# Performance work log

Measured on AMD Instinct MI355X. Metric: run time of the kernel, lower is better.

The kernel has to match this reference:

```python
import jax, jax.numpy as jnp
import numpy as np

N = 131072          # number of items ranked in one soft_rank call
CAPACITY = 3.0      # self.capcity in the torch module


def _pav_kl(y, w):
    """KL isotonic regression (non-increasing fit) via Pool-Adjacent-Violators.
    Pooled block value = logsumexp(y_block) - logsumexp(w_block).
    Matches torchsort / fast-soft-sort isotonic_kl. Sequential O(N)."""
    n = y.shape[0]

    def push(i, st):
        ly, lw, val, start, ptr = st
        ly = ly.at[ptr].set(y[i])
        lw = lw.at[ptr].set(w[i])
        val = val.at[ptr].set(y[i] - w[i])
        start = start.at[ptr].set(i)
        ptr = ptr + 1

        def cond(s):
            _, _, v, _, p = s
            return (p >= 2) & (v[p - 2] <= v[p - 1])

        def merge(s):
            ly, lw, v, stt, p = s
            ny = jnp.logaddexp(ly[p - 2], ly[p - 1])
            nw = jnp.logaddexp(lw[p - 2], lw[p - 1])
            return (ly.at[p - 2].set(ny), lw.at[p - 2].set(nw),
                    v.at[p - 2].set(ny - nw), stt, p - 1)

        return jax.lax.while_loop(cond, merge, (ly, lw, val, start, ptr))

    z = jnp.zeros((n,), y.dtype)
    st0 = (z, z, z, jnp.full((n,), n, jnp.int32), jnp.int32(0))
    ly, lw, val, start, ptr = jax.lax.fori_loop(0, n, push, st0)
    # invalidate stale stack slots, then map each element to its block value
    start = jnp.where(jnp.arange(n) < ptr, start, n)
    blk = jnp.searchsorted(start, jnp.arange(n), side='right') - 1
    return val[blk]


@jax.custom_vjp
def isotonic_kl(y, w):
    return _pav_kl(y, w)


def _iso_fwd(y, w):
    sol = _pav_kl(y, w)
    return sol, (y, w, sol)


def _iso_bwd(res, g):
    y, w, sol = res
    n = y.shape[0]
    # blocks = maximal runs of constant solution (exact equality by construction)
    blk = jnp.cumsum(jnp.concatenate([jnp.array([True]), sol[1:] != sol[:-1]])) - 1
    gsum = jax.ops.segment_sum(g, blk, num_segments=n)

    def seg_softmax(v):
        m = jax.ops.segment_max(v, blk, num_segments=n)
        lse = jnp.log(jax.ops.segment_sum(jnp.exp(v - m[blk]), blk, num_segments=n)) + m
        return jnp.exp(v - lse[blk])

    return seg_softmax(y) * gsum[blk], -seg_softmax(w) * gsum[blk]


isotonic_kl.defvjp(_iso_fwd, _iso_bwd)


def soft_rank_kl(scores):
    """torchsort.soft_rank(scores[None], regularization='kl'), strength=1, ascending."""
    n = scores.shape[0]
    w_log = jnp.log(jnp.arange(n, 0, -1, dtype=scores.dtype))  # log([n, ..., 1])
    perm = jnp.argsort(-scores)          # descending, stable
    s = scores[perm]
    sol = isotonic_kl(s, w_log)
    inv = jnp.argsort(perm)
    return jnp.exp(s - sol)[inv]


def setup_inputs() -> dict:
    key = jax.random.key(0)
    k = jax.random.split(key, 5)
    x = jax.random.normal(k[0], (N, 1), jnp.float32)
    # torch Linear default init bounds: 1/sqrt(fan_in)
    w1 = jax.random.uniform(k[1], (1, 32), jnp.float32, -1.0, 1.0)
    b1 = jax.random.uniform(k[2], (32,), jnp.float32, -1.0, 1.0)
    lim2 = 1.0 / np.sqrt(32.0)
    w2 = jax.random.uniform(k[3], (32, 1), jnp.float32, -lim2, lim2)
    b2 = jax.random.uniform(k[4], (1,), jnp.float32, -lim2, lim2)
    return {"x": x, "w1": w1, "b1": b1, "w2": w2, "b2": b2}


def reference(x, w1, b1, w2, b2):
    h = jnp.maximum(x @ w1 + b1, 0.0)            # [N, 32]
    scores = (h @ w2 + b2).reshape(-1)           # [N]
    ranks = soft_rank_kl(scores)                 # [N]
    other = jax.lax.stop_gradient(ranks) % CAPACITY
    ranks = (ranks - other) / CAPACITY + 1.0
    return ranks.reshape(-1, 1)
```

## Files before the change

kernel.cpp:

```cpp
#include <hip/hip_runtime.h>
#include <stdint.h>

typedef unsigned int u32;
typedef unsigned long long u64;

#define N_ITEMS 131072
#define NB 131072
#define NSLICE 4
#define MBLK 64
#define BUCK_PER_BLK 2048
#define CH_PER_BLK 32
#define PAD 65
#define REGSLOT 2048
#define FIXSCALE 268435456.0f
#define FIXMASK ((1ull << 46) - 1)


__device__ __forceinline__ float wsumf(int s, int e) {
  return 0.5f * (float)(e - s + 1) * (float)(2 * N_ITEMS - s - e);
}

__device__ __forceinline__ float key_to_score(u32 key) {
  u32 m = ~key;
  u32 u = (m & 0x80000000u) ? (m ^ 0x80000000u) : ~m;
  return __uint_as_float(u);
}

#define LOG2E 1.4426950408889634f
__device__ __forceinline__ float fexp(float x) { return exp2f(x * LOG2E); }

__device__ __forceinline__ u32 bucket_of(u32 key, u32 kmin, u32 kmax) {
  double scale = (double)NB / ((double)(kmax - kmin) + 1.0);
  u32 b = (u32)((double)(key - kmin) * scale);
  return b < NB ? b : (NB - 1);
}

__device__ __forceinline__ float recSY(int2 r) { return __int_as_float(r.y); }


__global__ __launch_bounds__(256) void score_key_kernel(
    const float* __restrict__ x,
    const float* __restrict__ w1, const float* __restrict__ b1,
    const float* __restrict__ w2, const float* __restrict__ b2,
    u32* __restrict__ keyRaw, u32* __restrict__ agg) {
  __shared__ u32 wmn[4], wmx[4];
  int t = threadIdx.x;
  int i = blockIdx.x * 256 + t;
  float xv = x[i];
  float s = b2[0];
#pragma unroll
  for (int j = 0; j < 32; ++j) {
    float h = fmaf(xv, w1[j], b1[j]);
    h = fmaxf(h, 0.0f);
    s = fmaf(h, w2[j], s);
  }
  u32 u = __float_as_uint(s);
  u32 m = u ^ ((u & 0x80000000u) ? 0xFFFFFFFFu : 0x80000000u);
  u32 key = ~m;
  keyRaw[i] = key;
  u32 mn = key, mx = key;
#pragma unroll
  for (int off = 32; off > 0; off >>= 1) {
    mn = min(mn, (u32)__shfl_xor((int)mn, off));
    mx = max(mx, (u32)__shfl_xor((int)mx, off));
  }
  if ((t & 63) == 0) { wmn[t >> 6] = mn; wmx[t >> 6] = mx; }
  __syncthreads();
  if (t == 0) {
    mn = min(min(wmn[0], wmn[1]), min(wmn[2], wmn[3]));
    mx = max(max(wmx[0], wmx[1]), max(wmx[2], wmx[3]));
    atomicMax(&agg[0], ~mn);
    atomicMax(&agg[1], mx);
  }
}


__global__ __launch_bounds__(256) void hist_kernel(
    const u32* __restrict__ keyRaw, const u32* __restrict__ agg,
    u64* __restrict__ hist8) {
  int t = threadIdx.x;
  int i = blockIdx.x * 256 + t;
  u32 kmin = ~agg[0], kmax = agg[1];
  u32 key = keyRaw[i];
  u32 g = bucket_of(key, kmin, kmax);
  float smax = key_to_score(kmin);
  float v = fexp(key_to_score(key) - smax);
  u64 fix = (u64)fmaxf(1.0f, fmaf(v, FIXSCALE, 0.5f));
  size_t slice = (size_t)(blockIdx.x & (NSLICE - 1)) * NB;
  atomicAdd(&hist8[slice + g], (1ull << 46) | fix);
}


__global__ __launch_bounds__(256) void solve_kernel(
    const u64* __restrict__ hist8, u64* __restrict__ flags, u64* __restrict__ flag2,
    u32* __restrict__ cdf, int2* __restrict__ REC,
    const u32* __restrict__ keyRaw, const u32* __restrict__ agg,
    float* __restrict__ out) {
  __shared__ u32 vals[BUCK_PER_BLK + 1];
  __shared__ float seL[BUCK_PER_BLK];
  __shared__ int   rST[CH_PER_BLK * PAD];
  __shared__ float rSY[CH_PER_BLK * PAD];
  __shared__ u32 sh[256];
  __shared__ u32 aggS[64];
  __shared__ u32 regS[65];
  __shared__ int lcnt[CH_PER_BLK];
  __shared__ int ca[16], cb[16], cM[16];
  __shared__ int shInt[4];
  int t = threadIdx.x, b = blockIdx.x;
  int B0 = b * BUCK_PER_BLK;
  for (int q = 0; q < 8; ++q) {
    int ii = q * 256 + t;
    u64 acc = 0;
#pragma unroll
    for (int c = 0; c < NSLICE; ++c) acc += hist8[(size_t)c * NB + B0 + ii];
    vals[ii] = (u32)(acc >> 46);
    seL[ii] = (float)(acc & FIXMASK) * (1.0f / FIXSCALE);
  }
  __syncthreads();
  u32 loc[8]; u32 s = 0;
  for (int q = 0; q < 8; ++q) { loc[q] = s; s += vals[t * 8 + q]; }
  sh[t] = s;
  __syncthreads();
  for (int off = 1; off < 256; off <<= 1) {
    u32 x2 = (t >= off) ? sh[t - off] : 0u;
    __syncthreads();
    sh[t] += x2;
    __syncthreads();
  }
  if (t == 0) atomicExch(&flags[b], (1ull << 32) | (u64)sh[255]);
  if (t < 64) {
    u64 f;
    do { f = atomicAdd(&flags[t], 0ull); } while ((u32)(f >> 32) == 0u);
    aggS[t] = (u32)f;
  }
  __syncthreads();
  if (t < 64) {
    u32 v = aggS[t];
    u32 inc = v;
    for (int off = 1; off < 64; off <<= 1) {
      u32 o2 = __shfl_up(inc, off);
      if (t >= off) inc += o2;
    }
    regS[t] = inc - v;
    if (t == 63) regS[64] = inc;
  }
  __syncthreads();
  u32 exclu = regS[b];
  u32 tbase = ((t == 0) ? 0u : sh[t - 1]) + exclu;
  u32 eb8[8];
  for (int q = 0; q < 8; ++q) { eb8[q] = tbase + loc[q]; vals[t * 8 + q] = eb8[q]; }
  {
    uint4* c4 = (uint4*)(cdf + B0 + t * 8);
    c4[0] = make_uint4(eb8[0], eb8[1], eb8[2], eb8[3]);
    c4[1] = make_uint4(eb8[4], eb8[5], eb8[6], eb8[7]);
  }
  if (t == 255) vals[BUCK_PER_BLK] = exclu + sh[255];
  __syncthreads();
  if (t < CH_PER_BLK) {
    int base = t * PAD;
    int ptr = 0; bool have = false;
    float syT = 0.0f; int stT = 0;
    for (int k = 0; k < 64; ++k) {
      u32 cs = vals[t * 64 + k], ce = vals[t * 64 + k + 1];
      if (ce == cs) continue;
      float syC = seL[t * 64 + k];
      int stC = (int)cs, eC = (int)ce - 1;
      while (have) {
        float SWc = wsumf(stC, eC);
        float SWt = wsumf(stT, stC - 1);
        if (!(syT * SWc <= syC * SWt)) break;
        syC += syT; stC = stT;
        if (ptr == 0) { have = false; break; }
        --ptr;
        stT = rST[base + ptr]; syT = rSY[base + ptr];
      }
      if (have) { rST[base + ptr] = stT; rSY[base + ptr] = syT; ++ptr; }
      stT = stC; syT = syC; have = true;
    }
    if (have) { rST[base + ptr] = stT; rSY[base + ptr] = syT; ++ptr; }
    lcnt[t] = ptr;
  }
  __syncthreads();
  for (int j = 0; j < 5; ++j) {
    int P = CH_PER_BLK >> (j + 1);
    if (t < P) {
      int p = t;
      int kL = p << (j + 1), kR = kL + (1 << j);
      int slotL = kL * PAD, slotR = kR * PAD;
      int nL = lcnt[kL], nR = lcnt[kR];
      int a = 0, bb = 0, hasM = 0;
      if (nL > 0 && nR > 0) {
        int gstartR = (int)vals[kR * 64];
        int gendR   = (int)vals[(kR + (1 << j)) * 64];
        float SYL = rSY[slotL + nL - 1]; int stL = rST[slotL + nL - 1];
        float SYR = rSY[slotR];
        int eR = (nR > 1) ? (rST[slotR + 1] - 1) : (gendR - 1);
        float SWL = wsumf(stL, gstartR - 1);
        float SWR = wsumf(gstartR, eR);
        if (SYL * SWR <= SYR * SWL) {
          hasM = 1;
          float SYM = SYL + SYR; int Ms = stL, Me = eR;
          a = 1; bb = 1;
          for (;;) {
            float SWM = wsumf(Ms, Me);
            if (a < nL) {
              float SYe = rSY[slotL + nL - 1 - a]; int ste = rST[slotL + nL - 1 - a];
              float SWe = wsumf(ste, Ms - 1);
              if (SYe * SWM <= SYM * SWe) { SYM += SYe; Ms = ste; ++a; continue; }
            }
            if (bb < nR) {
              float SYb = rSY[slotR + bb]; int sb = rST[slotR + bb];
              int eb = (bb + 1 < nR) ? (rST[slotR + bb + 1] - 1) : (gendR - 1);
              float SWb = wsumf(sb, eb);
              if (SYM * SWb <= SYb * SWM) { SYM += SYb; Me = eb; ++bb; continue; }
            }
            break;
          }
          rST[slotL + nL - a] = Ms; rSY[slotL + nL - a] = SYM;
        }
      }
      ca[p] = a; cb[p] = bb; cM[p] = hasM;
    }
    __syncthreads();
    {
      int w = t >> 6, lane = t & 63;
      for (int p = w; p < P; p += 4) {
        int kL = p << (j + 1), kR = kL + (1 << j);
        int nL = lcnt[kL], nR = lcnt[kR];
        int a = ca[p], bb = cb[p], hasM = cM[p];
        int destBase = kL * PAD + nL - a + hasM;
        int srcBase = kR * PAD + bb;
        int ncopy = nR - bb;
        for (int off = 0; off < ncopy; off += 64) {
          int k2 = off + lane; bool act = k2 < ncopy;
          int vt = 0; float vs = 0.f;
          if (act) { vt = rST[srcBase + k2]; vs = rSY[srcBase + k2]; }
          if (act) { rST[destBase + k2] = vt; rSY[destBase + k2] = vs; }
        }
      }
    }
    __syncthreads();
    if (t < P) {
      int p = t; int kL = p << (j + 1), kR = kL + (1 << j);
      lcnt[kL] = lcnt[kL] - ca[p] + cM[p] + (lcnt[kR] - cb[p]);
    }
    __syncthreads();
  }
  int myCnt = lcnt[0];
  for (int k = t; k < myCnt; k += 256)
    REC[(size_t)b * REGSLOT + k] = make_int2(rST[k], __float_as_int(rSY[k]));
  __syncthreads();
  int lvl = 0;
  for (;;) {
    if (b & (1 << lvl)) {
      __threadfence();
      if (t == 0) atomicExch(&flag2[b], (1ull << 32) | (u64)(u32)myCnt);
      break;
    }
    if (lvl == 6) {
      __threadfence();
      if (t == 0) atomicExch(&flag2[0], (2ull << 32) | (u64)(u32)myCnt);
      break;
    }
    int pb = b + (1 << lvl);
    if (t == 0) {
      u64 f;
      do { f = atomicAdd(&flag2[pb], 0ull); __builtin_amdgcn_s_sleep(1); } while ((f >> 32) == 0ull);
      shInt[0] = (int)(u32)f;
    }
    __syncthreads();
    __threadfence();
    int nR = shInt[0];
    int nL = myCnt;
    int slotL = b * REGSLOT, slotR = pb * REGSLOT;
    if (t == 0) {
      int a = 0, bb = 0, hasM = 0;
      if (nL > 0 && nR > 0) {
        int gstartR = (int)regS[pb];
        int gendR   = (int)regS[b + (2 << lvl)];
        int2 rL = REC[slotL + nL - 1];
        float SYL = recSY(rL); int stL = rL.x;
        int2 rR = REC[slotR];
        float SYR = recSY(rR);
        int eR = (nR > 1) ? (REC[slotR + 1].x - 1) : (gendR - 1);
        float SWL = wsumf(stL, gstartR - 1);
        float SWR = wsumf(gstartR, eR);
        if (SYL * SWR <= SYR * SWL) {
          hasM = 1;
          float SYM = SYL + SYR; int Ms = stL, Me = eR;
          a = 1; bb = 1;
          for (;;) {
            float SWM = wsumf(Ms, Me);
            if (a < nL) {
              int2 re = REC[slotL + nL - 1 - a];
              float SYe = recSY(re); int ste = re.x;
              float SWe = wsumf(ste, Ms - 1);
              if (SYe * SWM <= SYM * SWe) { SYM += SYe; Ms = ste; ++a; continue; }
            }
            if (bb < nR) {
              int2 rb = REC[slotR + bb];
              float SYb = recSY(rb); int sb = rb.x;
              int eb = (bb + 1 < nR) ? (REC[slotR + bb + 1].x - 1) : (gendR - 1);
              float SWb = wsumf(sb, eb);
              if (SYM * SWb <= SYb * SWM) { SYM += SYb; Me = eb; ++bb; continue; }
            }
            break;
          }
          REC[slotL + nL - a] = make_int2(Ms, __float_as_int(SYM));
        }
      }
      shInt[1] = a; shInt[2] = bb; shInt[3] = hasM;
    }
    __syncthreads();
    int a = shInt[1], bb = shInt[2], hasM = shInt[3];
    int destBase = slotL + nL - a + hasM;
    int srcBase = slotR + bb;
    int ncopy = nR - bb;
    for (int off = 0; off < ncopy; off += 256) {
      int k2 = off + t; bool act = k2 < ncopy;
      int2 vr = make_int2(0, 0);
      if (act) vr = REC[srcBase + k2];
      __syncthreads();
      if (act) REC[destBase + k2] = vr;
      __syncthreads();
    }
    __syncthreads();
    myCnt = nL - a + hasM + (nR - bb);
    ++lvl;
  }
  if (t == 0) {
    u64 f;
    do { f = atomicAdd(&flag2[0], 0ull); __builtin_amdgcn_s_sleep(2); } while ((f >> 32) != 2ull);
    shInt[0] = (int)(u32)f;
  }
  __syncthreads();
  __threadfence();
  int m = shInt[0];
  bool useL = (m <= CH_PER_BLK * PAD);
  if (useL) {
    for (int k = t; k < m; k += 256) {
      int2 r = REC[k];
      rST[k] = r.x; rSY[k] = __int_as_float(r.y);
    }
  }
  __syncthreads();
  u32 kmin = ~agg[0], kmax = agg[1];
  float smax = key_to_score(kmin);
  for (int q = 0; q < 8; ++q) {
    int i = b * 2048 + q * 256 + t;
    u32 key = keyRaw[i];
    u32 g = bucket_of(key, kmin, kmax);
    int p = (int)cdf[g];
    int lo = 0, hi = m - 1;
    if (useL) {
      while (lo < hi) {
        int mid = (lo + hi + 1) >> 1;
        if (rST[mid] <= p) lo = mid; else hi = mid - 1;
      }
      int s0 = rST[lo];
      int e0 = (lo + 1 < m) ? (rST[lo + 1] - 1) : (N_ITEMS - 1);
      float SW = wsumf(s0, e0);
      float sc = key_to_score(key);
      float rank = fexp(sc - smax) * SW / rSY[lo];
      out[i] = floorf(rank * (1.0f / 3.0f)) + 1.0f;
    } else {
      while (lo < hi) {
        int mid = (lo + hi + 1) >> 1;
        if (REC[mid].x <= p) lo = mid; else hi = mid - 1;
      }
      int2 r = REC[lo];
      int s0 = r.x;
      int e0 = (lo + 1 < m) ? (REC[lo + 1].x - 1) : (N_ITEMS - 1);
      float SW = wsumf(s0, e0);
      float sc = key_to_score(key);
      float rank = fexp(sc - smax) * SW / recSY(r);
      out[i] = floorf(rank * (1.0f / 3.0f)) + 1.0f;
    }
  }
}


extern "C" void kernel_launch(void* const* d_in, const int* in_sizes, int n_in,
                              void* d_out, int out_size, void* d_ws, size_t ws_size,
                              hipStream_t stream) {
  const float* x  = (const float*)d_in[0];
  const float* w1 = (const float*)d_in[1];
  const float* b1 = (const float*)d_in[2];
  const float* w2 = (const float*)d_in[3];
  const float* b2 = (const float*)d_in[4];
  float* out = (float*)d_out;

  char* ws = (char*)d_ws;
  size_t o = 0;
  u32* cdf    = (u32*)(ws + o); o += (size_t)(NB + 4) * 4;
  u32* keyRaw = (u32*)(ws + o); o += (size_t)N_ITEMS * 4;
  int2* REC   = (int2*)(ws + o); o += (size_t)N_ITEMS * 8;
  char* zbase = ws + o;
  u64* hist8  = (u64*)(ws + o); o += (size_t)NSLICE * NB * 8;
  u64* flags  = (u64*)(ws + o); o += (size_t)MBLK * 8;
  u64* flag2  = (u64*)(ws + o); o += (size_t)MBLK * 8;
  u32* agg    = (u32*)(ws + o); o += 64;
  size_t zbytes = (size_t)((ws + o) - zbase);

  hipMemsetAsync(zbase, 0, zbytes, stream);
  score_key_kernel<<<512, 256, 0, stream>>>(x, w1, b1, w2, b2, keyRaw, agg);
  hist_kernel<<<512, 256, 0, stream>>>(keyRaw, agg, hist8);
  solve_kernel<<<MBLK, 256, 0, stream>>>(hist8, flags, flag2, cdf, REC, keyRaw, agg, out);
}
```

Measured before the change: 142.9 us.

## Pad spin flags, use relaxed atomic loads, cache merge boundary records in LDS

```diff
diff --git a/kernel.cpp b/kernel.cpp
--- a/kernel.cpp
+++ b/kernel.cpp
@@ -12,6 +12,7 @@
 #define CH_PER_BLK 32
 #define PAD 65
 #define REGSLOT 2048
+#define FPAD 16
 #define FIXSCALE 268435456.0f
 #define FIXMASK ((1ull << 46) - 1)
 
@@ -37,15 +38,24 @@
 
 __device__ __forceinline__ float recSY(int2 r) { return __int_as_float(r.y); }
 
+__device__ __forceinline__ u64 agent_ld(const u64* p) {
+  return __hip_atomic_load(p, __ATOMIC_RELAXED, __HIP_MEMORY_SCOPE_AGENT);
+}
+
 
 __global__ __launch_bounds__(256) void score_key_kernel(
     const float* __restrict__ x,
     const float* __restrict__ w1, const float* __restrict__ b1,
     const float* __restrict__ w2, const float* __restrict__ b2,
-    u32* __restrict__ keyRaw, u32* __restrict__ agg) {
+    u32* __restrict__ keyRaw, u32* __restrict__ agg, u64* __restrict__ hist8) {
   __shared__ u32 wmn[4], wmx[4];
   int t = threadIdx.x;
   int i = blockIdx.x * 256 + t;
+  {
+    uint4 z = make_uint4(0u, 0u, 0u, 0u);
+    ((uint4*)hist8)[i] = z;
+    ((uint4*)hist8)[i + N_ITEMS] = z;
+  }
   float xv = x[i];
   float s = b2[0];
 #pragma unroll
@@ -127,10 +137,10 @@
     sh[t] += x2;
     __syncthreads();
   }
-  if (t == 0) atomicExch(&flags[b], (1ull << 32) | (u64)sh[255]);
+  if (t == 0) atomicExch(&flags[(size_t)b * FPAD], (1ull << 32) | (u64)sh[255]);
   if (t < 64) {
     u64 f;
-    do { f = atomicAdd(&flags[t], 0ull); } while ((u32)(f >> 32) == 0u);
+    do { f = agent_ld(&flags[(size_t)t * FPAD]); } while ((u32)(f >> 32) == 0u);
     aggS[t] = (u32)f;
   }
   __syncthreads();
@@ -250,11 +260,19 @@
   for (int k = t; k < myCnt; k += 256)
     REC[(size_t)b * REGSLOT + k] = make_int2(rST[k], __float_as_int(rSY[k]));
   __syncthreads();
+#define LRECC(idx_, st_, sy_) { int _a = (idx_); \
+    if (_a < 128) { st_ = rST[_a]; sy_ = rSY[_a]; } \
+    else { int2 _r = REC[slotL + nL - 1 - _a]; st_ = _r.x; sy_ = __int_as_float(_r.y); } }
+#define RRECC(idx_, st_, sy_) { int _i = (idx_); \
+    if (_i < 128) { st_ = rST[128 + _i]; sy_ = rSY[128 + _i]; } \
+    else { int2 _r = REC[slotR + _i]; st_ = _r.x; sy_ = __int_as_float(_r.y); } }
+#define RSTC(idx_, st_) { int _i = (idx_); \
+    if (_i < 128) { st_ = rST[128 + _i]; } else { st_ = REC[slotR + _i].x; } }
   int lvl = 0;
   for (;;) {
     if (b & (1 << lvl)) {
       __threadfence();
-      if (t == 0) atomicExch(&flag2[b], (1ull << 32) | (u64)(u32)myCnt);
+      if (t == 0) atomicExch(&flag2[(size_t)b * FPAD], (1ull << 32) | (u64)(u32)myCnt);
       break;
     }
     if (lvl == 6) {
@@ -263,26 +281,34 @@
       break;
     }
     int pb = b + (1 << lvl);
+    int nL = myCnt;
+    int slotL = b * REGSLOT, slotR = pb * REGSLOT;
+    if (t >= 64 && t < 192) {
+      int p2 = t - 64;
+      if (p2 < nL) { int2 r = REC[slotL + nL - 1 - p2]; rST[p2] = r.x; rSY[p2] = __int_as_float(r.y); }
+    }
     if (t == 0) {
       u64 f;
-      do { f = atomicAdd(&flag2[pb], 0ull); __builtin_amdgcn_s_sleep(1); } while ((f >> 32) == 0ull);
+      do { f = agent_ld(&flag2[(size_t)pb * FPAD]); __builtin_amdgcn_s_sleep(1); } while ((f >> 32) == 0ull);
       shInt[0] = (int)(u32)f;
     }
     __syncthreads();
     __threadfence();
     int nR = shInt[0];
-    int nL = myCnt;
-    int slotL = b * REGSLOT, slotR = pb * REGSLOT;
+    if (t >= 64 && t < 192) {
+      int p2 = t - 64;
+      if (p2 < nR) { int2 r = REC[slotR + p2]; rST[128 + p2] = r.x; rSY[128 + p2] = __int_as_float(r.y); }
+    }
+    __syncthreads();
     if (t == 0) {
       int a = 0, bb = 0, hasM = 0;
       if (nL > 0 && nR > 0) {
         int gstartR = (int)regS[pb];
         int gendR   = (int)regS[b + (2 << lvl)];
-        int2 rL = REC[slotL + nL - 1];
-        float SYL = recSY(rL); int stL = rL.x;
-        int2 rR = REC[slotR];
-        float SYR = recSY(rR);
-        int eR = (nR > 1) ? (REC[slotR + 1].x - 1) : (gendR - 1);
+        int stL; float SYL; LRECC(0, stL, SYL);
+        int sb0; float SYR; RRECC(0, sb0, SYR); (void)sb0;
+        int eR;
+        if (nR > 1) { int nx; RSTC(1, nx); eR = nx - 1; } else eR = gendR - 1;
         float SWL = wsumf(stL, gstartR - 1);
         float SWR = wsumf(gstartR, eR);
         if (SYL * SWR <= SYR * SWL) {
@@ -292,15 +318,14 @@
           for (;;) {
             float SWM = wsumf(Ms, Me);
             if (a < nL) {
-              int2 re = REC[slotL + nL - 1 - a];
-              float SYe = recSY(re); int ste = re.x;
+              int ste; float SYe; LRECC(a, ste, SYe);
               float SWe = wsumf(ste, Ms - 1);
               if (SYe * SWM <= SYM * SWe) { SYM += SYe; Ms = ste; ++a; continue; }
             }
             if (bb < nR) {
-              int2 rb = REC[slotR + bb];
-              float SYb = recSY(rb); int sb = rb.x;
-              int eb = (bb + 1 < nR) ? (REC[slotR + bb + 1].x - 1) : (gendR - 1);
+              int sb; float SYb; RRECC(bb, sb, SYb);
+              int eb;
+              if (bb + 1 < nR) { int nx; RSTC(bb + 1, nx); eb = nx - 1; } else eb = gendR - 1;
               float SWb = wsumf(sb, eb);
               if (SYM * SWb <= SYb * SWM) { SYM += SYb; Me = eb; ++bb; continue; }
             }
@@ -316,21 +341,33 @@
     int destBase = slotL + nL - a + hasM;
     int srcBase = slotR + bb;
     int ncopy = nR - bb;
-    for (int off = 0; off < ncopy; off += 256) {
-      int k2 = off + t; bool act = k2 < ncopy;
-      int2 vr = make_int2(0, 0);
-      if (act) vr = REC[srcBase + k2];
-      __syncthreads();
-      if (act) REC[destBase + k2] = vr;
-      __syncthreads();
+    if (destBase != srcBase) {
+      for (int off = 0; off < ncopy; off += 2048) {
+        int2 v[8];
+#pragma unroll
+        for (int j = 0; j < 8; ++j) {
+          int k2 = off + j * 256 + t;
+          if (k2 < ncopy) v[j] = REC[srcBase + k2];
+        }
+        __syncthreads();
+#pragma unroll
+        for (int j = 0; j < 8; ++j) {
+          int k2 = off + j * 256 + t;
+          if (k2 < ncopy) REC[destBase + k2] = v[j];
+        }
+        __syncthreads();
+      }
     }
     __syncthreads();
     myCnt = nL - a + hasM + (nR - bb);
     ++lvl;
   }
+#undef LRECC
+#undef RRECC
+#undef RSTC
   if (t == 0) {
     u64 f;
-    do { f = atomicAdd(&flag2[0], 0ull); __builtin_amdgcn_s_sleep(2); } while ((f >> 32) != 2ull);
+    do { f = agent_ld(&flag2[0]); __builtin_amdgcn_s_sleep(2); } while ((f >> 32) != 2ull);
     shInt[0] = (int)(u32)f;
   }
   __syncthreads();
@@ -395,15 +432,15 @@
   u32* cdf    = (u32*)(ws + o); o += (size_t)(NB + 4) * 4;
   u32* keyRaw = (u32*)(ws + o); o += (size_t)N_ITEMS * 4;
   int2* REC   = (int2*)(ws + o); o += (size_t)N_ITEMS * 8;
+  u64* hist8  = (u64*)(ws + o); o += (size_t)NSLICE * NB * 8;
   char* zbase = ws + o;
-  u64* hist8  = (u64*)(ws + o); o += (size_t)NSLICE * NB * 8;
-  u64* flags  = (u64*)(ws + o); o += (size_t)MBLK * 8;
-  u64* flag2  = (u64*)(ws + o); o += (size_t)MBLK * 8;
+  u64* flags  = (u64*)(ws + o); o += (size_t)MBLK * FPAD * 8;
+  u64* flag2  = (u64*)(ws + o); o += (size_t)MBLK * FPAD * 8;
   u32* agg    = (u32*)(ws + o); o += 64;
   size_t zbytes = (size_t)((ws + o) - zbase);
 
   hipMemsetAsync(zbase, 0, zbytes, stream);
-  score_key_kernel<<<512, 256, 0, stream>>>(x, w1, b1, w2, b2, keyRaw, agg);
+  score_key_kernel<<<512, 256, 0, stream>>>(x, w1, b1, w2, b2, keyRaw, agg, hist8);
   hist_kernel<<<512, 256, 0, stream>>>(keyRaw, agg, hist8);
   solve_kernel<<<MBLK, 256, 0, stream>>>(hist8, flags, flag2, cdf, REC, keyRaw, agg, out);
 }
```

New measurement: 139.4 us. 1.03x faster.

## Split solve into scan, grouped merge and output kernels; drop memset and atomics

Applied to the files above, without the earlier changes.

```diff
diff --git a/kernel.cpp b/kernel.cpp
--- a/kernel.cpp
+++ b/kernel.cpp
@@ -12,6 +12,7 @@
 #define CH_PER_BLK 32
 #define PAD 65
 #define REGSLOT 2048
+#define FPAD 16
 #define FIXSCALE 268435456.0f
 #define FIXMASK ((1ull << 46) - 1)
 
@@ -37,15 +38,90 @@
 
 __device__ __forceinline__ float recSY(int2 r) { return __int_as_float(r.y); }
 
+__device__ __forceinline__ u64 agent_ld(const u64* p) {
+  return __hip_atomic_load(p, __ATOMIC_RELAXED, __HIP_MEMORY_SCOPE_AGENT);
+}
+
+__device__ int merge_step(int2* __restrict__ REC, int slotL, int nL,
+                          int slotR, int nR, int gstartR, int gendR,
+                          int t, int* shInt) {
+  if (t == 0) {
+    int a = 0, bb = 0, hasM = 0;
+    if (nL > 0 && nR > 0) {
+      int2 rL = REC[slotL + nL - 1];
+      float SYL = recSY(rL); int stL = rL.x;
+      int2 rR = REC[slotR];
+      float SYR = recSY(rR);
+      int eR = (nR > 1) ? (REC[slotR + 1].x - 1) : (gendR - 1);
+      float SWL = wsumf(stL, gstartR - 1);
+      float SWR = wsumf(gstartR, eR);
+      if (SYL * SWR <= SYR * SWL) {
+        hasM = 1;
+        float SYM = SYL + SYR; int Ms = stL, Me = eR;
+        a = 1; bb = 1;
+        for (;;) {
+          float SWM = wsumf(Ms, Me);
+          if (a < nL) {
+            int2 re = REC[slotL + nL - 1 - a];
+            float SYe = recSY(re); int ste = re.x;
+            float SWe = wsumf(ste, Ms - 1);
+            if (SYe * SWM <= SYM * SWe) { SYM += SYe; Ms = ste; ++a; continue; }
+          }
+          if (bb < nR) {
+            int2 rb = REC[slotR + bb];
+            float SYb = recSY(rb); int sb = rb.x;
+            int eb = (bb + 1 < nR) ? (REC[slotR + bb + 1].x - 1) : (gendR - 1);
+            float SWb = wsumf(sb, eb);
+            if (SYM * SWb <= SYb * SWM) { SYM += SYb; Me = eb; ++bb; continue; }
+          }
+          break;
+        }
+        REC[slotL + nL - a] = make_int2(Ms, __float_as_int(SYM));
+      }
+    }
+    shInt[0] = a; shInt[1] = bb; shInt[2] = hasM;
+  }
+  __syncthreads();
+  int a = shInt[0], bb = shInt[1], hasM = shInt[2];
+  int destBase = slotL + nL - a + hasM;
+  int srcBase = slotR + bb;
+  int ncopy = nR - bb;
+  if (destBase != srcBase) {
+    for (int off = 0; off < ncopy; off += 2048) {
+      int2 v[8];
+#pragma unroll
+      for (int j = 0; j < 8; ++j) {
+        int k2 = off + j * 256 + t;
+        if (k2 < ncopy) v[j] = REC[srcBase + k2];
+      }
+      __syncthreads();
+#pragma unroll
+      for (int j = 0; j < 8; ++j) {
+        int k2 = off + j * 256 + t;
+        if (k2 < ncopy) REC[destBase + k2] = v[j];
+      }
+      __syncthreads();
+    }
+  }
+  __syncthreads();
+  return nL - a + hasM + ncopy;
+}
+
 
 __global__ __launch_bounds__(256) void score_key_kernel(
     const float* __restrict__ x,
     const float* __restrict__ w1, const float* __restrict__ b1,
     const float* __restrict__ w2, const float* __restrict__ b2,
-    u32* __restrict__ keyRaw, u32* __restrict__ agg) {
+    u32* __restrict__ keyRaw, u32* __restrict__ pmin, u32* __restrict__ pmax,
+    u64* __restrict__ hist8, u64* __restrict__ flags, u64* __restrict__ grpf) {
   __shared__ u32 wmn[4], wmx[4];
   int t = threadIdx.x;
   int i = blockIdx.x * 256 + t;
+  uint4 z = make_uint4(0u, 0u, 0u, 0u);
+  ((uint4*)hist8)[i] = z;
+  ((uint4*)hist8)[i + N_ITEMS] = z;
+  if (i < MBLK) flags[(size_t)i * FPAD] = 0ull;
+  if (i < 9) grpf[(size_t)i * FPAD] = 0ull;
   float xv = x[i];
   float s = b2[0];
 #pragma unroll
@@ -69,18 +145,28 @@
   if (t == 0) {
     mn = min(min(wmn[0], wmn[1]), min(wmn[2], wmn[3]));
     mx = max(max(wmx[0], wmx[1]), max(wmx[2], wmx[3]));
-    atomicMax(&agg[0], ~mn);
-    atomicMax(&agg[1], mx);
+    pmin[blockIdx.x] = mn;
+    pmax[blockIdx.x] = mx;
   }
 }
 
 
 __global__ __launch_bounds__(256) void hist_kernel(
-    const u32* __restrict__ keyRaw, const u32* __restrict__ agg,
-    u64* __restrict__ hist8) {
+    const u32* __restrict__ keyRaw,
+    const u32* __restrict__ pmin, const u32* __restrict__ pmax,
+    u64* __restrict__ hist8, u32* __restrict__ mm) {
+  __shared__ u32 s0[256], s1[256];
   int t = threadIdx.x;
+  s0[t] = min(pmin[t], pmin[t + 256]);
+  s1[t] = max(pmax[t], pmax[t + 256]);
+  __syncthreads();
+  for (int off = 128; off > 0; off >>= 1) {
+    if (t < off) { s0[t] = min(s0[t], s0[t + off]); s1[t] = max(s1[t], s1[t + off]); }
+    __syncthreads();
+  }
+  u32 kmin = s0[0], kmax = s1[0];
+  if (blockIdx.x == 0 && t == 0) { mm[0] = kmin; mm[1] = kmax; }
   int i = blockIdx.x * 256 + t;
-  u32 kmin = ~agg[0], kmax = agg[1];
   u32 key = keyRaw[i];
   u32 g = bucket_of(key, kmin, kmax);
   float smax = key_to_score(kmin);
@@ -91,21 +177,18 @@
 }
 
 
-__global__ __launch_bounds__(256) void solve_kernel(
-    const u64* __restrict__ hist8, u64* __restrict__ flags, u64* __restrict__ flag2,
+__global__ __launch_bounds__(256) void scan_pav_kernel(
+    const u64* __restrict__ hist8, u64* __restrict__ flags,
     u32* __restrict__ cdf, int2* __restrict__ REC,
-    const u32* __restrict__ keyRaw, const u32* __restrict__ agg,
-    float* __restrict__ out) {
+    int* __restrict__ cnt2, u32* __restrict__ rstart) {
   __shared__ u32 vals[BUCK_PER_BLK + 1];
   __shared__ float seL[BUCK_PER_BLK];
   __shared__ int   rST[CH_PER_BLK * PAD];
   __shared__ float rSY[CH_PER_BLK * PAD];
-  __shared__ u32 sh[256];
-  __shared__ u32 aggS[64];
+  __shared__ u32 wsum[4];
   __shared__ u32 regS[65];
   __shared__ int lcnt[CH_PER_BLK];
   __shared__ int ca[16], cb[16], cM[16];
-  __shared__ int shInt[4];
   int t = threadIdx.x, b = blockIdx.x;
   int B0 = b * BUCK_PER_BLK;
   for (int q = 0; q < 8; ++q) {
@@ -119,34 +202,37 @@
   __syncthreads();
   u32 loc[8]; u32 s = 0;
   for (int q = 0; q < 8; ++q) { loc[q] = s; s += vals[t * 8 + q]; }
-  sh[t] = s;
-  __syncthreads();
-  for (int off = 1; off < 256; off <<= 1) {
-    u32 x2 = (t >= off) ? sh[t - off] : 0u;
-    __syncthreads();
-    sh[t] += x2;
-    __syncthreads();
-  }
-  if (t == 0) atomicExch(&flags[b], (1ull << 32) | (u64)sh[255]);
+  u32 inc = s;
+#pragma unroll
+  for (int off = 1; off < 64; off <<= 1) {
+    u32 o2 = (u32)__shfl_up((int)inc, off);
+    if ((t & 63) >= off) inc += o2;
+  }
+  if ((t & 63) == 63) wsum[t >> 6] = inc;
+  __syncthreads();
+  u32 w = (u32)(t >> 6);
+  u32 woff = 0;
+  if (w > 0) woff += wsum[0];
+  if (w > 1) woff += wsum[1];
+  if (w > 2) woff += wsum[2];
+  u32 total = wsum[0] + wsum[1] + wsum[2] + wsum[3];
+  u32 texcl = woff + inc - s;
+  if (t == 0) atomicExch(&flags[(size_t)b * FPAD], (1ull << 32) | (u64)total);
   if (t < 64) {
     u64 f;
-    do { f = atomicAdd(&flags[t], 0ull); } while ((u32)(f >> 32) == 0u);
-    aggS[t] = (u32)f;
-  }
-  __syncthreads();
-  if (t < 64) {
-    u32 v = aggS[t];
-    u32 inc = v;
+    do { f = agent_ld(&flags[(size_t)t * FPAD]); } while ((u32)(f >> 32) == 0u);
+    u32 v = (u32)f, inc2 = v;
+#pragma unroll
     for (int off = 1; off < 64; off <<= 1) {
-      u32 o2 = __shfl_up(inc, off);
-      if (t >= off) inc += o2;
-    }
-    regS[t] = inc - v;
-    if (t == 63) regS[64] = inc;
+      u32 o2 = (u32)__shfl_up((int)inc2, off);
+      if (t >= off) inc2 += o2;
+    }
+    regS[t] = inc2 - v;
+    if (t == 63) regS[64] = inc2;
   }
   __syncthreads();
   u32 exclu = regS[b];
-  u32 tbase = ((t == 0) ? 0u : sh[t - 1]) + exclu;
+  u32 tbase = texcl + exclu;
   u32 eb8[8];
   for (int q = 0; q < 8; ++q) { eb8[q] = tbase + loc[q]; vals[t * 8 + q] = eb8[q]; }
   {
@@ -154,7 +240,8 @@
     c4[0] = make_uint4(eb8[0], eb8[1], eb8[2], eb8[3]);
     c4[1] = make_uint4(eb8[4], eb8[5], eb8[6], eb8[7]);
   }
-  if (t == 255) vals[BUCK_PER_BLK] = exclu + sh[255];
+  if (t == 255) vals[BUCK_PER_BLK] = exclu + total;
+  if (b == 0 && t < 65) rstart[t] = regS[t];
   __syncthreads();
   if (t < CH_PER_BLK) {
     int base = t * PAD;
@@ -223,8 +310,8 @@
     }
     __syncthreads();
     {
-      int w = t >> 6, lane = t & 63;
-      for (int p = w; p < P; p += 4) {
+      int wv = t >> 6, lane = t & 63;
+      for (int p = wv; p < P; p += 4) {
         int kL = p << (j + 1), kR = kL + (1 << j);
         int nL = lcnt[kL], nR = lcnt[kR];
         int a = ca[p], bb = cb[p], hasM = cM[p];
@@ -246,96 +333,66 @@
     }
     __syncthreads();
   }
-  int myCnt = lcnt[0];
-  for (int k = t; k < myCnt; k += 256)
+  int n = lcnt[0];
+  for (int k = t; k < n; k += 256)
     REC[(size_t)b * REGSLOT + k] = make_int2(rST[k], __float_as_int(rSY[k]));
-  __syncthreads();
-  int lvl = 0;
-  for (;;) {
-    if (b & (1 << lvl)) {
-      __threadfence();
-      if (t == 0) atomicExch(&flag2[b], (1ull << 32) | (u64)(u32)myCnt);
-      break;
-    }
-    if (lvl == 6) {
-      __threadfence();
-      if (t == 0) atomicExch(&flag2[0], (2ull << 32) | (u64)(u32)myCnt);
-      break;
-    }
-    int pb = b + (1 << lvl);
-    if (t == 0) {
+  if (t == 0) cnt2[b] = n;
+}
+
+
+__global__ __launch_bounds__(256) void merge_kernel(
+    int2* __restrict__ REC, int* __restrict__ cnt2,
+    const u32* __restrict__ rstart, u64* __restrict__ grpf) {
+  __shared__ int shInt[4];
+  __shared__ int gcnt[8];
+  __shared__ u32 rs[65];
+  __shared__ int pcnt[8];
+  int t = threadIdx.x, b = blockIdx.x;
+  if (t < 8) gcnt[t] = cnt2[b * 8 + t];
+  if (t < 65) rs[t] = rstart[t];
+  __syncthreads();
+  int nL = gcnt[0];
+  int slotL = (b * 8) * REGSLOT;
+  for (int k = 1; k < 8; ++k) {
+    int nR = gcnt[k];
+    int slotR = (b * 8 + k) * REGSLOT;
+    nL = merge_step(REC, slotL, nL, slotR, nR,
+                    (int)rs[b * 8 + k], (int)rs[b * 8 + k + 1], t, shInt);
+  }
+  if (t == 0) { __threadfence(); atomicExch(&grpf[(size_t)b * FPAD], (1ull << 32) | (u64)(u32)nL); }
+  if (b == 0) {
+    if (t < 7) {
       u64 f;
-      do { f = atomicAdd(&flag2[pb], 0ull); __builtin_amdgcn_s_sleep(1); } while ((f >> 32) == 0ull);
-      shInt[0] = (int)(u32)f;
+      do { f = agent_ld(&grpf[(size_t)(1 + t) * FPAD]); } while ((u32)(f >> 32) == 0u);
+      pcnt[1 + t] = (int)(u32)f;
     }
     __syncthreads();
     __threadfence();
-    int nR = shInt[0];
-    int nL = myCnt;
-    int slotL = b * REGSLOT, slotR = pb * REGSLOT;
-    if (t == 0) {
-      int a = 0, bb = 0, hasM = 0;
-      if (nL > 0 && nR > 0) {
-        int gstartR = (int)regS[pb];
-        int gendR   = (int)regS[b + (2 << lvl)];
-        int2 rL = REC[slotL + nL - 1];
-        float SYL = recSY(rL); int stL = rL.x;
-        int2 rR = REC[slotR];
-        float SYR = recSY(rR);
-        int eR = (nR > 1) ? (REC[slotR + 1].x - 1) : (gendR - 1);
-        float SWL = wsumf(stL, gstartR - 1);
-        float SWR = wsumf(gstartR, eR);
-        if (SYL * SWR <= SYR * SWL) {
-          hasM = 1;
-          float SYM = SYL + SYR; int Ms = stL, Me = eR;
-          a = 1; bb = 1;
-          for (;;) {
-            float SWM = wsumf(Ms, Me);
-            if (a < nL) {
-              int2 re = REC[slotL + nL - 1 - a];
-              float SYe = recSY(re); int ste = re.x;
-              float SWe = wsumf(ste, Ms - 1);
-              if (SYe * SWM <= SYM * SWe) { SYM += SYe; Ms = ste; ++a; continue; }
-            }
-            if (bb < nR) {
-              int2 rb = REC[slotR + bb];
-              float SYb = recSY(rb); int sb = rb.x;
-              int eb = (bb + 1 < nR) ? (REC[slotR + bb + 1].x - 1) : (gendR - 1);
-              float SWb = wsumf(sb, eb);
-              if (SYM * SWb <= SYb * SWM) { SYM += SYb; Me = eb; ++bb; continue; }
-            }
-            break;
-          }
-          REC[slotL + nL - a] = make_int2(Ms, __float_as_int(SYM));
-        }
-      }
-      shInt[1] = a; shInt[2] = bb; shInt[3] = hasM;
-    }
-    __syncthreads();
-    int a = shInt[1], bb = shInt[2], hasM = shInt[3];
-    int destBase = slotL + nL - a + hasM;
-    int srcBase = slotR + bb;
-    int ncopy = nR - bb;
-    for (int off = 0; off < ncopy; off += 256) {
-      int k2 = off + t; bool act = k2 < ncopy;
-      int2 vr = make_int2(0, 0);
-      if (act) vr = REC[srcBase + k2];
-      __syncthreads();
-      if (act) REC[destBase + k2] = vr;
-      __syncthreads();
-    }
-    __syncthreads();
-    myCnt = nL - a + hasM + (nR - bb);
-    ++lvl;
-  }
-  if (t == 0) {
-    u64 f;
-    do { f = atomicAdd(&flag2[0], 0ull); __builtin_amdgcn_s_sleep(2); } while ((f >> 32) != 2ull);
-    shInt[0] = (int)(u32)f;
-  }
-  __syncthreads();
-  __threadfence();
-  int m = shInt[0];
+    for (int k = 1; k < 8; ++k) {
+      int nR = pcnt[k];
+      int slotR = (k * 8) * REGSLOT;
+      nL = merge_step(REC, 0, nL, slotR, nR,
+                      (int)rs[k * 8], (int)rs[k * 8 + 8], t, shInt);
+    }
+    if (t == 0) cnt2[0] = nL;
+  }
+}
+
+
+__global__ __launch_bounds__(256) void out_kernel(
+    const u32* __restrict__ keyRaw, const u32* __restrict__ mm,
+    const u32* __restrict__ cdf, const int2* __restrict__ REC,
+    const int* __restrict__ cnt2, float* __restrict__ out) {
+  __shared__ int   rST[CH_PER_BLK * PAD];
+  __shared__ float rSY[CH_PER_BLK * PAD];
+  int t = threadIdx.x;
+  int i = blockIdx.x * 256 + t;
+  int m = cnt2[0];
+  u32 kmin = mm[0], kmax = mm[1];
+  u32 key = keyRaw[i];
+  float smax = key_to_score(kmin);
+  u32 g = bucket_of(key, kmin, kmax);
+  int p = (int)cdf[g];
   bool useL = (m <= CH_PER_BLK * PAD);
   if (useL) {
     for (int k = t; k < m; k += 256) {
@@ -344,38 +401,28 @@
     }
   }
   __syncthreads();
-  u32 kmin = ~agg[0], kmax = agg[1];
-  float smax = key_to_score(kmin);
-  for (int q = 0; q < 8; ++q) {
-    int i = b * 2048 + q * 256 + t;
-    u32 key = keyRaw[i];
-    u32 g = bucket_of(key, kmin, kmax);
-    int p = (int)cdf[g];
-    int lo = 0, hi = m - 1;
-    if (useL) {
-      while (lo < hi) {
-        int mid = (lo + hi + 1) >> 1;
-        if (rST[mid] <= p) lo = mid; else hi = mid - 1;
-      }
-      int s0 = rST[lo];
-      int e0 = (lo + 1 < m) ? (rST[lo + 1] - 1) : (N_ITEMS - 1);
-      float SW = wsumf(s0, e0);
-      float sc = key_to_score(key);
-      float rank = fexp(sc - smax) * SW / rSY[lo];
-      out[i] = floorf(rank * (1.0f / 3.0f)) + 1.0f;
-    } else {
-      while (lo < hi) {
-        int mid = (lo + hi + 1) >> 1;
-        if (REC[mid].x <= p) lo = mid; else hi = mid - 1;
-      }
-      int2 r = REC[lo];
-      int s0 = r.x;
-      int e0 = (lo + 1 < m) ? (REC[lo + 1].x - 1) : (N_ITEMS - 1);
-      float SW = wsumf(s0, e0);
-      float sc = key_to_score(key);
-      float rank = fexp(sc - smax) * SW / recSY(r);
-      out[i] = floorf(rank * (1.0f / 3.0f)) + 1.0f;
-    }
+  int lo = 0, hi = m - 1;
+  if (useL) {
+    while (lo < hi) {
+      int mid = (lo + hi + 1) >> 1;
+      if (rST[mid] <= p) lo = mid; else hi = mid - 1;
+    }
+    int s0 = rST[lo];
+    int e0 = (lo + 1 < m) ? (rST[lo + 1] - 1) : (N_ITEMS - 1);
+    float SW = wsumf(s0, e0);
+    float rank = fexp(key_to_score(key) - smax) * SW / rSY[lo];
+    out[i] = floorf(rank * (1.0f / 3.0f)) + 1.0f;
+  } else {
+    while (lo < hi) {
+      int mid = (lo + hi + 1) >> 1;
+      if (REC[mid].x <= p) lo = mid; else hi = mid - 1;
+    }
+    int2 r = REC[lo];
+    int s0 = r.x;
+    int e0 = (lo + 1 < m) ? (REC[lo + 1].x - 1) : (N_ITEMS - 1);
+    float SW = wsumf(s0, e0);
+    float rank = fexp(key_to_score(key) - smax) * SW / recSY(r);
+    out[i] = floorf(rank * (1.0f / 3.0f)) + 1.0f;
   }
 }
 
@@ -392,18 +439,22 @@
 
   char* ws = (char*)d_ws;
   size_t o = 0;
+  u32* mm     = (u32*)(ws + o); o += 64;
+  u32* pmin   = (u32*)(ws + o); o += (size_t)512 * 4;
+  u32* pmax   = (u32*)(ws + o); o += (size_t)512 * 4;
   u32* cdf    = (u32*)(ws + o); o += (size_t)(NB + 4) * 4;
+  u32* rstart = (u32*)(ws + o); o += (size_t)(MBLK + 4) * 4;
   u32* keyRaw = (u32*)(ws + o); o += (size_t)N_ITEMS * 4;
   int2* REC   = (int2*)(ws + o); o += (size_t)N_ITEMS * 8;
-  char* zbase = ws + o;
+  int* cnt2   = (int*)(ws + o);  o += (size_t)MBLK * 4;
   u64* hist8  = (u64*)(ws + o); o += (size_t)NSLICE * NB * 8;
-  u64* flags  = (u64*)(ws + o); o += (size_t)MBLK * 8;
-  u64* flag2  = (u64*)(ws + o); o += (size_t)MBLK * 8;
-  u32* agg    = (u32*)(ws + o); o += 64;
-  size_t zbytes = (size_t)((ws + o) - zbase);
-
-  hipMemsetAsync(zbase, 0, zbytes, stream);
-  score_key_kernel<<<512, 256, 0, stream>>>(x, w1, b1, w2, b2, keyRaw, agg);
-  hist_kernel<<<512, 256, 0, stream>>>(keyRaw, agg, hist8);
-  solve_kernel<<<MBLK, 256, 0, stream>>>(hist8, flags, flag2, cdf, REC, keyRaw, agg, out);
-}
+  u64* flags  = (u64*)(ws + o); o += (size_t)MBLK * FPAD * 8;
+  u64* grpf   = (u64*)(ws + o); o += (size_t)9 * FPAD * 8;
+
+  score_key_kernel<<<512, 256, 0, stream>>>(x, w1, b1, w2, b2, keyRaw,
+                                            pmin, pmax, hist8, flags, grpf);
+  hist_kernel<<<512, 256, 0, stream>>>(keyRaw, pmin, pmax, hist8, mm);
+  scan_pav_kernel<<<MBLK, 256, 0, stream>>>(hist8, flags, cdf, REC, cnt2, rstart);
+  merge_kernel<<<8, 256, 0, stream>>>(REC, cnt2, rstart, grpf);
+  out_kernel<<<512, 256, 0, stream>>>(keyRaw, mm, cdf, REC, cnt2, out);
+}
```

New measurement: 116.8 us. -18.2%, faster.
